# Performance work log

Measured on AMD Instinct MI355X. Metric: run time of the kernel, lower is better.

Reference implementation:

```python
import jax, jax.numpy as jnp
import numpy as np

B, T, F_IN = 256, 168, 128
H = 512            # encoder hidden per direction; decoder hidden = 2H
OUT = 1
L_OUT = 48
SCALE = 0.05


def _lstm_scan(x, Wih, Whh, b, h0, c0):
    # x: [T, B, F]; PyTorch LSTM gate order i, f, g, o
    def step(carry, xt):
        h, c = carry
        g = xt @ Wih.T + h @ Whh.T + b
        i, f, gg, o = jnp.split(g, 4, axis=-1)
        c = jax.nn.sigmoid(f) * c + jax.nn.sigmoid(i) * jnp.tanh(gg)
        h = jax.nn.sigmoid(o) * jnp.tanh(c)
        return (h, c), h
    (hT, cT), ys = jax.lax.scan(step, (h0, c0), x)
    return ys, hT, cT


def setup_inputs() -> dict:
    key = jax.random.key(0)
    ks = jax.random.split(key, 16)
    r = lambda k, shp: (jax.random.normal(k, shp, dtype=jnp.float32) * SCALE)
    return {
        "input_seq": jax.random.normal(ks[0], (B, T, F_IN), dtype=jnp.float32),
        "enc_Wih_f": r(ks[1], (4 * H, F_IN)),
        "enc_Whh_f": r(ks[2], (4 * H, H)),
        "enc_bih_f": r(ks[3], (4 * H,)),
        "enc_bhh_f": r(ks[4], (4 * H,)),
        "enc_Wih_b": r(ks[5], (4 * H, F_IN)),
        "enc_Whh_b": r(ks[6], (4 * H, H)),
        "enc_bih_b": r(ks[7], (4 * H,)),
        "enc_bhh_b": r(ks[8], (4 * H,)),
        "dec_Wih": r(ks[9], (4 * 2 * H, OUT)),
        "dec_Whh": r(ks[10], (4 * 2 * H, 2 * H)),
        "dec_bih": r(ks[11], (4 * 2 * H,)),
        "dec_bhh": r(ks[12], (4 * 2 * H,)),
        "fc_W": r(ks[13], (OUT, 2 * H)),
        "fc_b": r(ks[14], (OUT,)),
        "output_length": L_OUT,
    }


def reference(input_seq, enc_Wih_f, enc_Whh_f, enc_bih_f, enc_bhh_f,
              enc_Wih_b, enc_Whh_b, enc_bih_b, enc_bhh_b,
              dec_Wih, dec_Whh, dec_bih, dec_bhh, fc_W, fc_b, output_length):
    b = input_seq.shape[0]
    h = enc_Whh_f.shape[1]
    x = jnp.transpose(input_seq, (1, 0, 2))  # [T, B, F]
    h0 = jnp.zeros((b, h), input_seq.dtype)
    c0 = jnp.zeros((b, h), input_seq.dtype)
    # bidirectional encoder (final hidden/cell only are used downstream)
    _, hf, cf = _lstm_scan(x, enc_Wih_f, enc_Whh_f, enc_bih_f + enc_bhh_f, h0, c0)
    _, hb, cb = _lstm_scan(x[::-1], enc_Wih_b, enc_Whh_b, enc_bih_b + enc_bhh_b, h0, c0)
    # _cat_hidden: concat fwd/bwd states along feature dim -> decoder init state [B, 2H]
    hd = jnp.concatenate([hf, hb], axis=-1)
    cd = jnp.concatenate([cf, cb], axis=-1)
    bd = dec_bih + dec_bhh
    x0 = jnp.zeros((b, fc_W.shape[0]), input_seq.dtype)  # initial decoder input = zeros

    def dec_step(carry, _):
        hh, cc, xt = carry
        g = xt @ dec_Wih.T + hh @ dec_Whh.T + bd
        i, f, gg, o = jnp.split(g, 4, axis=-1)
        cc = jax.nn.sigmoid(f) * cc + jax.nn.sigmoid(i) * jnp.tanh(gg)
        hh = jax.nn.sigmoid(o) * jnp.tanh(cc)
        pred = hh @ fc_W.T + fc_b  # [B, OUT]
        return (hh, cc, pred), pred

    _, preds = jax.lax.scan(dec_step, (hd, cd, x0), None, length=output_length)
    # [L, B, OUT] -> [B, L, OUT] -> squeeze(dim=2) with OUT==1 -> [B, L]
    return jnp.transpose(preds, (1, 0, 2)).squeeze(2)
```

## Files before the change

### kernel.cpp

```cpp
#include <hip/hip_runtime.h>


constexpr int B_ = 256, T_ = 168, F_ = 128, H_ = 512, L_ = 48;
constexpr int KE = F_ + H_;
constexpr int HD = 1024;
constexpr int GE = 4 * H_;
constexpr int GD = 4 * HD;
constexpr int EPAD = KE + 8;
constexpr int DPAD = HD + 8;

constexpr int GBAR_IDX = 0;
constexpr int CLAIM_IDX = 64;
constexpr int ENCF_IDX = 640;
constexpr int DECF_IDX = 1280;

constexpr size_t OFF_SYNC = 0;
constexpr size_t OFF_WCF = 8192;
constexpr size_t OFF_WCB = OFF_WCF + (size_t)GE * KE * 2;
constexpr size_t OFF_WD  = OFF_WCB + (size_t)GE * KE * 2;
constexpr size_t OFF_BF  = OFF_WD  + (size_t)GD * HD * 2;
constexpr size_t OFF_BB  = OFF_BF  + (size_t)GE * 4;
constexpr size_t OFF_BD  = OFF_BB  + (size_t)GE * 4;
constexpr size_t OFF_WIH = OFF_BD  + (size_t)GD * 4;
constexpr size_t OFF_XH  = OFF_WIH + (size_t)GD * 4;
constexpr size_t OFF_HE  = OFF_XH  + (size_t)T_ * B_ * F_ * 2;
constexpr size_t OFF_HDD = OFF_HE  + (size_t)2 * 2 * B_ * H_ * 2;
constexpr size_t OFF_CD  = OFF_HDD + (size_t)2 * B_ * HD * 2;

using h8 = __attribute__((ext_vector_type(8))) _Float16;
using f4 = __attribute__((ext_vector_type(4))) float;

#define DEV static __device__ __forceinline__

DEV float sigm(float x)  { return __fdividef(1.f, 1.f + __expf(-x)); }
DEV float tanh_(float x) { return 1.f - __fdividef(2.f, __expf(2.f * x) + 1.f); }

DEV h8 as_h8(f4 v) { union { f4 f; h8 h; } u; u.f = v; return u.h; }

DEV void astore_u64(void* p, unsigned long long v) {
  __hip_atomic_store((unsigned long long*)p, v, __ATOMIC_RELAXED,
                     __HIP_MEMORY_SCOPE_AGENT);
}
DEV void astore_u32(void* p, unsigned v) {
  __hip_atomic_store((unsigned*)p, v, __ATOMIC_RELAXED, __HIP_MEMORY_SCOPE_AGENT);
}
DEV unsigned aload_u32(const void* p) {
  return __hip_atomic_load((const unsigned*)p, __ATOMIC_RELAXED,
                           __HIP_MEMORY_SCOPE_AGENT);
}
DEV float aload_f32(const void* p) {
  return __hip_atomic_load((const float*)p, __ATOMIC_RELAXED,
                           __HIP_MEMORY_SCOPE_AGENT);
}
DEV void astore_f32(void* p, float v) {
  __hip_atomic_store((float*)p, v, __ATOMIC_RELAXED, __HIP_MEMORY_SCOPE_AGENT);
}
DEV void vm_drain() { asm volatile("s_waitcnt vmcnt(0)" ::: "memory"); }

template<bool DEEP>
DEV void ld16(const _Float16* p, f4* A) {
#define L16(FL) asm volatile( \
    "global_load_dwordx4 %0,  %16, off" FL "\n\t" \
    "global_load_dwordx4 %1,  %16, off offset:64" FL "\n\t" \
    "global_load_dwordx4 %2,  %16, off offset:128" FL "\n\t" \
    "global_load_dwordx4 %3,  %16, off offset:192" FL "\n\t" \
    "global_load_dwordx4 %4,  %16, off offset:256" FL "\n\t" \
    "global_load_dwordx4 %5,  %16, off offset:320" FL "\n\t" \
    "global_load_dwordx4 %6,  %16, off offset:384" FL "\n\t" \
    "global_load_dwordx4 %7,  %16, off offset:448" FL "\n\t" \
    "global_load_dwordx4 %8,  %16, off offset:512" FL "\n\t" \
    "global_load_dwordx4 %9,  %16, off offset:576" FL "\n\t" \
    "global_load_dwordx4 %10, %16, off offset:640" FL "\n\t" \
    "global_load_dwordx4 %11, %16, off offset:704" FL "\n\t" \
    "global_load_dwordx4 %12, %16, off offset:768" FL "\n\t" \
    "global_load_dwordx4 %13, %16, off offset:832" FL "\n\t" \
    "global_load_dwordx4 %14, %16, off offset:896" FL "\n\t" \
    "global_load_dwordx4 %15, %16, off offset:960" FL "\n\t" \
    "s_waitcnt vmcnt(0)" \
    : "=&v"(A[0]),"=&v"(A[1]),"=&v"(A[2]),"=&v"(A[3]),"=&v"(A[4]),"=&v"(A[5]), \
      "=&v"(A[6]),"=&v"(A[7]),"=&v"(A[8]),"=&v"(A[9]),"=&v"(A[10]),"=&v"(A[11]), \
      "=&v"(A[12]),"=&v"(A[13]),"=&v"(A[14]),"=&v"(A[15]) \
    : "v"(p) : "memory")
  if constexpr (DEEP) { L16(" sc0 sc1"); } else { L16(" sc0"); }
#undef L16
}

DEV void ld32(const _Float16* p, f4* A) {
  asm volatile(
    "global_load_dwordx4 %0,  %32, off sc0 sc1\n\t"
    "global_load_dwordx4 %1,  %32, off offset:64 sc0 sc1\n\t"
    "global_load_dwordx4 %2,  %32, off offset:128 sc0 sc1\n\t"
    "global_load_dwordx4 %3,  %32, off offset:192 sc0 sc1\n\t"
    "global_load_dwordx4 %4,  %32, off offset:256 sc0 sc1\n\t"
    "global_load_dwordx4 %5,  %32, off offset:320 sc0 sc1\n\t"
    "global_load_dwordx4 %6,  %32, off offset:384 sc0 sc1\n\t"
    "global_load_dwordx4 %7,  %32, off offset:448 sc0 sc1\n\t"
    "global_load_dwordx4 %8,  %32, off offset:512 sc0 sc1\n\t"
    "global_load_dwordx4 %9,  %32, off offset:576 sc0 sc1\n\t"
    "global_load_dwordx4 %10, %32, off offset:640 sc0 sc1\n\t"
    "global_load_dwordx4 %11, %32, off offset:704 sc0 sc1\n\t"
    "global_load_dwordx4 %12, %32, off offset:768 sc0 sc1\n\t"
    "global_load_dwordx4 %13, %32, off offset:832 sc0 sc1\n\t"
    "global_load_dwordx4 %14, %32, off offset:896 sc0 sc1\n\t"
    "global_load_dwordx4 %15, %32, off offset:960 sc0 sc1\n\t"
    "global_load_dwordx4 %16, %32, off offset:1024 sc0 sc1\n\t"
    "global_load_dwordx4 %17, %32, off offset:1088 sc0 sc1\n\t"
    "global_load_dwordx4 %18, %32, off offset:1152 sc0 sc1\n\t"
    "global_load_dwordx4 %19, %32, off offset:1216 sc0 sc1\n\t"
    "global_load_dwordx4 %20, %32, off offset:1280 sc0 sc1\n\t"
    "global_load_dwordx4 %21, %32, off offset:1344 sc0 sc1\n\t"
    "global_load_dwordx4 %22, %32, off offset:1408 sc0 sc1\n\t"
    "global_load_dwordx4 %23, %32, off offset:1472 sc0 sc1\n\t"
    "global_load_dwordx4 %24, %32, off offset:1536 sc0 sc1\n\t"
    "global_load_dwordx4 %25, %32, off offset:1600 sc0 sc1\n\t"
    "global_load_dwordx4 %26, %32, off offset:1664 sc0 sc1\n\t"
    "global_load_dwordx4 %27, %32, off offset:1728 sc0 sc1\n\t"
    "global_load_dwordx4 %28, %32, off offset:1792 sc0 sc1\n\t"
    "global_load_dwordx4 %29, %32, off offset:1856 sc0 sc1\n\t"
    "global_load_dwordx4 %30, %32, off offset:1920 sc0 sc1\n\t"
    "global_load_dwordx4 %31, %32, off offset:1984 sc0 sc1\n\t"
    "s_waitcnt vmcnt(0)"
    : "=&v"(A[0]),"=&v"(A[1]),"=&v"(A[2]),"=&v"(A[3]),"=&v"(A[4]),"=&v"(A[5]),
      "=&v"(A[6]),"=&v"(A[7]),"=&v"(A[8]),"=&v"(A[9]),"=&v"(A[10]),"=&v"(A[11]),
      "=&v"(A[12]),"=&v"(A[13]),"=&v"(A[14]),"=&v"(A[15]),"=&v"(A[16]),"=&v"(A[17]),
      "=&v"(A[18]),"=&v"(A[19]),"=&v"(A[20]),"=&v"(A[21]),"=&v"(A[22]),"=&v"(A[23]),
      "=&v"(A[24]),"=&v"(A[25]),"=&v"(A[26]),"=&v"(A[27]),"=&v"(A[28]),"=&v"(A[29]),
      "=&v"(A[30]),"=&v"(A[31])
    : "v"(p) : "memory");
}

DEV unsigned pollflag(const unsigned* p, bool deep) {
  unsigned v;
  if (deep)
    asm volatile("global_load_dword %0, %1, off sc0 sc1\n\t"
                 "s_waitcnt vmcnt(0)" : "=&v"(v) : "v"(p) : "memory");
  else
    asm volatile("global_load_dword %0, %1, off sc0\n\t"
                 "s_waitcnt vmcnt(0)" : "=&v"(v) : "v"(p) : "memory");
  return v;
}
DEV void wait_ge(const unsigned* p, unsigned target, bool deep, int cap) {
  for (int it = 0; it < cap; ++it) {
    unsigned v = pollflag(p, deep);
    if (__ballot(v >= target) == ~0ull) return;
  }
}

DEV void global_sync(unsigned* cnt, unsigned target) {
  vm_drain();
  __syncthreads();
  if (threadIdx.x == 0) {
    __hip_atomic_fetch_add(cnt, 1u, __ATOMIC_RELAXED, __HIP_MEMORY_SCOPE_AGENT);
    for (int it = 0; it < (1 << 20); ++it) {
      if (aload_u32(cnt) >= target) break;
    }
  }
  __syncthreads();
  asm volatile("" ::: "memory");
}

__global__ void prep_misc(const float* bihF, const float* bhhF,
                          const float* bihB, const float* bhhB,
                          const float* dbih, const float* dbhh,
                          const float* dwih, const float* fcb,
                          float* out, char* ws) {
  int i = blockIdx.x * blockDim.x + threadIdx.x;
  if (i < 1024) astore_u64(ws + (size_t)i * 8, 0ull);
  if (i < GE) {
    ((float*)(ws + OFF_BF))[i] = bihF[i] + bhhF[i];
    ((float*)(ws + OFF_BB))[i] = bihB[i] + bhhB[i];
  }
  if (i < GD) {
    ((float*)(ws + OFF_BD))[i]  = dbih[i] + dbhh[i];
    ((float*)(ws + OFF_WIH))[i] = dwih[i];
  }
  if (i < B_ * L_) out[i] = fcb[0];
  if (i < 2 * 2 * B_ * H_ / 4) astore_u64((char*)ws + OFF_HE + (size_t)i * 8, 0ull);
}

__global__ void conv_encw(const float* WihF, const float* WhhF,
                          const float* WihB, const float* WhhB, char* ws) {
  int i = blockIdx.x * blockDim.x + threadIdx.x;
  if (i >= GE * KE) return;
  int r = i / KE, k = i - r * KE;
  float vF = (k < F_) ? WihF[r * F_ + k] : WhhF[r * H_ + (k - F_)];
  float vB = (k < F_) ? WihB[r * F_ + k] : WhhB[r * H_ + (k - F_)];
  ((_Float16*)(ws + OFF_WCF))[i] = (_Float16)vF;
  ((_Float16*)(ws + OFF_WCB))[i] = (_Float16)vB;
}

__global__ void conv_decw(const float* W, char* ws) {
  int i = blockIdx.x * blockDim.x + threadIdx.x;
  if (i < GD * HD) ((_Float16*)(ws + OFF_WD))[i] = (_Float16)W[i];
}

__global__ void conv_x(const float* x, char* ws) {
  int i = blockIdx.x * blockDim.x + threadIdx.x;
  if (i >= T_ * B_ * F_) return;
  int f = i & 127, b = (i >> 7) & 255, t = i >> 15;
  ((_Float16*)(ws + OFF_XH))[i] = (_Float16)x[((size_t)b * T_ + t) * F_ + f];
}

template<bool LOCAL>
DEV void encoder_phase(int dir, int chunk, int slice,
                       int tid, int wave, int quad, int col, int lane,
                       char* ws, _Float16* lds, _Float16 (*htile)[16]) {
  const _Float16* Wenc  = (const _Float16*)(ws + (dir ? OFF_WCB : OFF_WCF));
  const float*    biasE = (const float*)(ws + (dir ? OFF_BB : OFF_BF));
  const _Float16* Xh    = (const _Float16*)(ws + OFF_XH);
  _Float16* hE = (_Float16*)(ws + OFF_HE);
  _Float16* hD = (_Float16*)(ws + OFF_HDD);
  float*    cD = (float*)(ws + OFF_CD);
  unsigned* encf = (unsigned*)ws + ENCF_IDX + (dir * 4 + chunk) * 64;

  const int j0 = slice * 16;
  const int mb = chunk * 64;

  for (int it = 0; it < 20; ++it) {
    int idx = it * 256 + tid;
    int n = idx / 80, e = idx - n * 80;
    int g = n >> 4, u = n & 15;
    *((h8*)(lds + n * EPAD) + e) =
        *((const h8*)(Wenc + (size_t)(g * H_ + j0 + u) * KE) + e);
  }
  float breg[4];
#pragma unroll
  for (int g = 0; g < 4; ++g) breg[g] = biasE[g * H_ + j0 + col];
  float cst[4] = {0.f, 0.f, 0.f, 0.f};
  __syncthreads();

  h8 Bf[4][16];
#pragma unroll
  for (int g = 0; g < 4; ++g)
#pragma unroll
    for (int kk = 0; kk < 16; ++kk)
      Bf[g][kk] = *((const h8*)(lds + (g * 16 + col) * EPAD + F_) + kk * 4 + quad);

  const int arow = mb + wave * 16 + col;
  const int mrow = mb + wave * 16 + quad * 4;

  for (int t = 0; t < T_; ++t) {
    const int par = t & 1;
    const int tx  = dir ? (T_ - 1 - t) : t;
    f4 z = {0.f, 0.f, 0.f, 0.f};
    f4 acc[4] = {z, z, z, z};

    const h8* xr = (const h8*)(Xh + ((size_t)tx * B_ + arow) * F_);
#pragma unroll
    for (int kk = 0; kk < 4; ++kk) {
      h8 a = xr[kk * 4 + quad];
#pragma unroll
      for (int g = 0; g < 4; ++g) {
        h8 b = *((const h8*)(lds + (g * 16 + col) * EPAD) + kk * 4 + quad);
        acc[g] = __builtin_amdgcn_mfma_f32_16x16x32_f16(a, b, acc[g], 0, 0, 0);
      }
    }
    if (t > 0)
      wait_ge(encf + (lane & 31), (unsigned)t, !LOCAL, 1 << 16);
    f4 A[16];
    ld16<!LOCAL>(hE + ((size_t)(par * 2 + dir) * B_ + arow) * H_ + quad * 8, A);
#pragma unroll
    for (int kk = 0; kk < 16; ++kk) {
      h8 a = as_h8(A[kk]);
#pragma unroll
      for (int g = 0; g < 4; ++g)
        acc[g] = __builtin_amdgcn_mfma_f32_16x16x32_f16(a, Bf[g][kk], acc[g], 0, 0, 0);
    }

#pragma unroll
    for (int r = 0; r < 4; ++r) {
      float gi = acc[0][r] + breg[0];
      float gf = acc[1][r] + breg[1];
      float gg = acc[2][r] + breg[2];
      float go = acc[3][r] + breg[3];
      float c = sigm(gf) * cst[r] + sigm(gi) * tanh_(gg);
      cst[r] = c;
      float h = sigm(go) * tanh_(c);
      htile[wave * 16 + quad * 4 + r][col] = (_Float16)h;
      if (t == T_ - 1)
        astore_f32(&cD[(size_t)(mrow + r) * HD + dir * H_ + j0 + col], c);
    }
    __syncthreads();
    if (tid < 128) {
      int row = tid >> 1, half = tid & 1;
      const unsigned long long* src =
          (const unsigned long long*)&htile[row][half * 8];
      if (t < T_ - 1) {
        _Float16* dst = hE + ((size_t)((par ^ 1) * 2 + dir) * B_ + mb + row) * H_ +
                        j0 + half * 8;
        if (LOCAL) {
          ((unsigned long long*)dst)[0] = src[0];
          ((unsigned long long*)(dst + 4))[0] = src[1];
        } else {
          astore_u64(dst, src[0]);
          astore_u64(dst + 4, src[1]);
        }
      } else {
        _Float16* dst = hD + (size_t)(mb + row) * HD + dir * H_ + j0 + half * 8;
        astore_u64(dst, src[0]);
        astore_u64(dst + 4, src[1]);
      }
    }
    vm_drain();
    __syncthreads();
    if (tid == 0 && t < T_ - 1) {
      if (LOCAL) *(volatile unsigned*)(encf + slice) = (unsigned)(t + 1);
      else       astore_u32(encf + slice, (unsigned)(t + 1));
    }
  }
}

DEV void decoder_phase(int slice, int chunk,
                       int tid, int wave, int quad, int col, int lane,
                       const float* fcW, float* out, char* ws,
                       _Float16* lds, _Float16 (*htile)[16]) {
  const _Float16* Wd    = (const _Float16*)(ws + OFF_WD);
  const float*    biasD = (const float*)(ws + OFF_BD);
  const float*    wihD  = (const float*)(ws + OFF_WIH);
  _Float16* hD = (_Float16*)(ws + OFF_HDD);
  float*    cD = (float*)(ws + OFF_CD);
  unsigned* decf = (unsigned*)ws + DECF_IDX + chunk * 64;

  const int j0 = slice * 16;
  const int mb = chunk * 64;

  for (int it = 0; it < 32; ++it) {
    int idx = it * 256 + tid;
    int n = idx >> 7, e = idx & 127;
    int g = n >> 4, u = n & 15;
    *((h8*)(lds + n * DPAD) + e) =
        *((const h8*)(Wd + (size_t)(g * HD + j0 + u) * HD) + e);
  }
  float breg[4], wreg[4];
#pragma unroll
  for (int g = 0; g < 4; ++g) {
    breg[g] = biasD[g * HD + j0 + col];
    wreg[g] = wihD[g * HD + j0 + col];
  }
  const float fcw = fcW[j0 + col];
  const int arow = mb + wave * 16 + col;
  const int mrow = mb + wave * 16 + quad * 4;
  float cst[4];
#pragma unroll
  for (int r = 0; r < 4; ++r)
    cst[r] = aload_f32(&cD[(size_t)(mrow + r) * HD + j0 + col]);
  __syncthreads();

  for (int l = 0; l < L_; ++l) {
    const int par = l & 1;
    if (l > 0) wait_ge(decf + lane, (unsigned)l, true, 1 << 16);
    f4 A[32];
    ld32(hD + ((size_t)par * B_ + arow) * HD + quad * 8, A);
    f4 z = {0.f, 0.f, 0.f, 0.f};
    f4 acc[4] = {z, z, z, z};
#pragma unroll
    for (int kk = 0; kk < 32; ++kk) {
      h8 a = as_h8(A[kk]);
#pragma unroll
      for (int g = 0; g < 4; ++g) {
        h8 b = *((const h8*)(lds + (g * 16 + col) * DPAD) + kk * 4 + quad);
        acc[g] = __builtin_amdgcn_mfma_f32_16x16x32_f16(a, b, acc[g], 0, 0, 0);
      }
    }
    float pr[4];
#pragma unroll
    for (int r = 0; r < 4; ++r)
      pr[r] = (l > 0) ? aload_f32(&out[(size_t)(mrow + r) * L_ + (l - 1)]) : 0.f;

    float sum[4];
#pragma unroll
    for (int r = 0; r < 4; ++r) {
      float gi = acc[0][r] + breg[0] + pr[r] * wreg[0];
      float gf = acc[1][r] + breg[1] + pr[r] * wreg[1];
      float gg = acc[2][r] + breg[2] + pr[r] * wreg[2];
      float go = acc[3][r] + breg[3] + pr[r] * wreg[3];
      float c = sigm(gf) * cst[r] + sigm(gi) * tanh_(gg);
      cst[r] = c;
      float h = sigm(go) * tanh_(c);
      htile[wave * 16 + quad * 4 + r][col] = (_Float16)h;
      sum[r] = h * fcw;
    }
#pragma unroll
    for (int off = 1; off < 16; off <<= 1) {
#pragma unroll
      for (int r = 0; r < 4; ++r) sum[r] += __shfl_xor(sum[r], off, 16);
    }
    if (col == 0) {
#pragma unroll
      for (int r = 0; r < 4; ++r)
        atomicAdd(&out[(size_t)(mrow + r) * L_ + l], sum[r]);
    }
    __syncthreads();
    if (l < L_ - 1 && tid < 128) {
      int row = tid >> 1, half = tid & 1;
      const unsigned long long* src =
          (const unsigned long long*)&htile[row][half * 8];
      _Float16* dst = hD + ((size_t)(par ^ 1) * B_ + mb + row) * HD +
                      j0 + half * 8;
      astore_u64(dst, src[0]);
      astore_u64(dst + 4, src[1]);
    }
    vm_drain();
    __syncthreads();
    if (tid == 0 && l < L_ - 1) astore_u32(decf + slice, (unsigned)(l + 1));
  }
}

__global__ __launch_bounds__(256, 1)
void rnn_kernel(const float* __restrict__ fcW, float* __restrict__ out,
                char* __restrict__ ws) {
  __shared__ __align__(16) _Float16 lds[64 * DPAD];
  __shared__ __align__(16) _Float16 htile[64][16];
  __shared__ int sh[2];

  const int tid  = threadIdx.x;
  const int wave = tid >> 6;
  const int lane = tid & 63;
  const int quad = lane >> 4;
  const int col  = lane & 15;
  const int bi   = blockIdx.x;

  unsigned* sync = (unsigned*)(ws + OFF_SYNC);
  unsigned* gbar = sync + GBAR_IDX;
  unsigned* claim = sync + CLAIM_IDX;

  if (tid == 0) {
    unsigned x;
    asm volatile("s_getreg_b32 %0, hwreg(HW_REG_XCC_ID)" : "=s"(x));
    int xcd = (int)(x & 7u);
    unsigned r = __hip_atomic_fetch_add(claim + xcd * 64, 1u, __ATOMIC_RELAXED,
                                        __HIP_MEMORY_SCOPE_AGENT);
    sh[0] = xcd;
    sh[1] = (int)r;
  }
  __syncthreads();
  const int xcd = sh[0], rank = sh[1];
  global_sync(gbar, 256u);
  if (tid == 0) {
    int d = 0;
    for (int k = 0; k < 8; ++k)
      if (aload_u32(claim + k * 64) != 32u) d = 1;
    sh[0] = d;
  }
  __syncthreads();
  const bool deg = (sh[0] != 0) || (rank >= 32);

  if (!deg)
    encoder_phase<true>(xcd >> 2, xcd & 3, rank, tid, wave, quad, col, lane,
                        ws, lds, htile);
  else
    encoder_phase<false>(bi >> 7, bi & 3, (bi & 127) >> 2, tid, wave, quad, col,
                         lane, ws, lds, htile);

  global_sync(gbar, 512u);

  decoder_phase(bi >> 2, bi & 3, tid, wave, quad, col, lane, fcW, out, ws, lds,
                htile);
}

extern "C" void kernel_launch(void* const* d_in, const int* in_sizes, int n_in,
                              void* d_out, int out_size, void* d_ws, size_t ws_size,
                              hipStream_t stream) {
  const float* x     = (const float*)d_in[0];
  const float* eWihF = (const float*)d_in[1];
  const float* eWhhF = (const float*)d_in[2];
  const float* ebihF = (const float*)d_in[3];
  const float* ebhhF = (const float*)d_in[4];
  const float* eWihB = (const float*)d_in[5];
  const float* eWhhB = (const float*)d_in[6];
  const float* ebihB = (const float*)d_in[7];
  const float* ebhhB = (const float*)d_in[8];
  const float* dWih  = (const float*)d_in[9];
  const float* dWhh  = (const float*)d_in[10];
  const float* dbih  = (const float*)d_in[11];
  const float* dbhh  = (const float*)d_in[12];
  const float* fcW   = (const float*)d_in[13];
  const float* fcb   = (const float*)d_in[14];
  float* out = (float*)d_out;
  char*  ws  = (char*)d_ws;

  prep_misc<<<2048, 256, 0, stream>>>(ebihF, ebhhF, ebihB, ebhhB, dbih, dbhh,
                                      dWih, fcb, out, ws);
  conv_encw<<<(GE * KE) / 256, 256, 0, stream>>>(eWihF, eWhhF, eWihB, eWhhB, ws);
  conv_decw<<<(GD * HD) / 256, 256, 0, stream>>>(dWhh, ws);
  conv_x<<<(T_ * B_ * F_) / 256, 256, 0, stream>>>(x, ws);

  void* args[] = {(void*)&fcW, (void*)&out, (void*)&ws};
  hipError_t err = hipLaunchCooperativeKernel(rnn_kernel, dim3(256), dim3(256),
                                              args, 0, stream);
  if (err != hipSuccess) {
    rnn_kernel<<<dim3(256), dim3(256), 0, stream>>>(fcW, out, ws);
  }
}
```

Measured before the change: 1.478 ms.

## Repartition decoder per XCD with in-register weights and partial-prediction exchange

The decoder is repartitioned so each XCD owns 32 batch rows and each block owns 32 hidden units. Half the gate weights are staged in LDS and half in registers, converted from fp32 inside the kernel, which removes the separate decoder weight conversion kernel and the bias prep. Predictions now come from per-block partial sums in a double-buffered buffer instead of global atomicAdds, and XCD-local flags replace the global per-chunk wait. The grid barrier changes from a shared atomic counter to per-block flags scanned with vector loads. The cost is more register pressure and a larger in-kernel weight load, and the LOCAL (non-coherent) path is never instantiated.

After: 1.476 ms. About the same (-0.2%).

```diff
diff --git a/kernel.cpp b/kernel.cpp
--- a/kernel.cpp
+++ b/kernel.cpp
@@ -5,30 +5,28 @@
 constexpr int KE = F_ + H_;
 constexpr int HD = 1024;
 constexpr int GE = 4 * H_;
-constexpr int GD = 4 * HD;
 constexpr int EPAD = KE + 8;
 constexpr int DPAD = HD + 8;
 
-constexpr int GBAR_IDX = 0;
-constexpr int CLAIM_IDX = 64;
-constexpr int ENCF_IDX = 640;
-constexpr int DECF_IDX = 1280;
+constexpr int FL256_IDX = 0;
+constexpr int CLAIM_IDX = 256;
+constexpr int ENCF_IDX  = 768;
+constexpr int DECF_IDX  = 1280;
 
 constexpr size_t OFF_SYNC = 0;
 constexpr size_t OFF_WCF = 8192;
 constexpr size_t OFF_WCB = OFF_WCF + (size_t)GE * KE * 2;
-constexpr size_t OFF_WD  = OFF_WCB + (size_t)GE * KE * 2;
-constexpr size_t OFF_BF  = OFF_WD  + (size_t)GD * HD * 2;
+constexpr size_t OFF_PP  = OFF_WCB + (size_t)GE * KE * 2;
+constexpr size_t OFF_BF  = OFF_PP  + (size_t)8 * 2 * 64 * 32 * 4;
 constexpr size_t OFF_BB  = OFF_BF  + (size_t)GE * 4;
-constexpr size_t OFF_BD  = OFF_BB  + (size_t)GE * 4;
-constexpr size_t OFF_WIH = OFF_BD  + (size_t)GD * 4;
-constexpr size_t OFF_XH  = OFF_WIH + (size_t)GD * 4;
+constexpr size_t OFF_XH  = OFF_BB  + (size_t)GE * 4;
 constexpr size_t OFF_HE  = OFF_XH  + (size_t)T_ * B_ * F_ * 2;
 constexpr size_t OFF_HDD = OFF_HE  + (size_t)2 * 2 * B_ * H_ * 2;
 constexpr size_t OFF_CD  = OFF_HDD + (size_t)2 * B_ * HD * 2;
 
 using h8 = __attribute__((ext_vector_type(8))) _Float16;
 using f4 = __attribute__((ext_vector_type(4))) float;
+using u4 = __attribute__((ext_vector_type(4))) unsigned;
 
 #define DEV static __device__ __forceinline__
 
@@ -54,6 +52,11 @@
 }
 DEV void astore_f32(void* p, float v) {
   __hip_atomic_store((float*)p, v, __ATOMIC_RELAXED, __HIP_MEMORY_SCOPE_AGENT);
+}
+DEV void astore_u16(void* p, _Float16 v) {
+  union { _Float16 h; unsigned short s; } u; u.h = v;
+  __hip_atomic_store((unsigned short*)p, u.s, __ATOMIC_RELAXED,
+                     __HIP_MEMORY_SCOPE_AGENT);
 }
 DEV void vm_drain() { asm volatile("s_waitcnt vmcnt(0)" ::: "memory"); }
 
@@ -85,48 +88,79 @@
 #undef L16
 }
 
+template<bool DEEP>
 DEV void ld32(const _Float16* p, f4* A) {
-  asm volatile(
-    "global_load_dwordx4 %0,  %32, off sc0 sc1\n\t"
-    "global_load_dwordx4 %1,  %32, off offset:64 sc0 sc1\n\t"
-    "global_load_dwordx4 %2,  %32, off offset:128 sc0 sc1\n\t"
-    "global_load_dwordx4 %3,  %32, off offset:192 sc0 sc1\n\t"
-    "global_load_dwordx4 %4,  %32, off offset:256 sc0 sc1\n\t"
-    "global_load_dwordx4 %5,  %32, off offset:320 sc0 sc1\n\t"
-    "global_load_dwordx4 %6,  %32, off offset:384 sc0 sc1\n\t"
-    "global_load_dwordx4 %7,  %32, off offset:448 sc0 sc1\n\t"
-    "global_load_dwordx4 %8,  %32, off offset:512 sc0 sc1\n\t"
-    "global_load_dwordx4 %9,  %32, off offset:576 sc0 sc1\n\t"
-    "global_load_dwordx4 %10, %32, off offset:640 sc0 sc1\n\t"
-    "global_load_dwordx4 %11, %32, off offset:704 sc0 sc1\n\t"
-    "global_load_dwordx4 %12, %32, off offset:768 sc0 sc1\n\t"
-    "global_load_dwordx4 %13, %32, off offset:832 sc0 sc1\n\t"
-    "global_load_dwordx4 %14, %32, off offset:896 sc0 sc1\n\t"
-    "global_load_dwordx4 %15, %32, off offset:960 sc0 sc1\n\t"
-    "global_load_dwordx4 %16, %32, off offset:1024 sc0 sc1\n\t"
-    "global_load_dwordx4 %17, %32, off offset:1088 sc0 sc1\n\t"
-    "global_load_dwordx4 %18, %32, off offset:1152 sc0 sc1\n\t"
-    "global_load_dwordx4 %19, %32, off offset:1216 sc0 sc1\n\t"
-    "global_load_dwordx4 %20, %32, off offset:1280 sc0 sc1\n\t"
-    "global_load_dwordx4 %21, %32, off offset:1344 sc0 sc1\n\t"
-    "global_load_dwordx4 %22, %32, off offset:1408 sc0 sc1\n\t"
-    "global_load_dwordx4 %23, %32, off offset:1472 sc0 sc1\n\t"
-    "global_load_dwordx4 %24, %32, off offset:1536 sc0 sc1\n\t"
-    "global_load_dwordx4 %25, %32, off offset:1600 sc0 sc1\n\t"
-    "global_load_dwordx4 %26, %32, off offset:1664 sc0 sc1\n\t"
-    "global_load_dwordx4 %27, %32, off offset:1728 sc0 sc1\n\t"
-    "global_load_dwordx4 %28, %32, off offset:1792 sc0 sc1\n\t"
-    "global_load_dwordx4 %29, %32, off offset:1856 sc0 sc1\n\t"
-    "global_load_dwordx4 %30, %32, off offset:1920 sc0 sc1\n\t"
-    "global_load_dwordx4 %31, %32, off offset:1984 sc0 sc1\n\t"
-    "s_waitcnt vmcnt(0)"
-    : "=&v"(A[0]),"=&v"(A[1]),"=&v"(A[2]),"=&v"(A[3]),"=&v"(A[4]),"=&v"(A[5]),
-      "=&v"(A[6]),"=&v"(A[7]),"=&v"(A[8]),"=&v"(A[9]),"=&v"(A[10]),"=&v"(A[11]),
-      "=&v"(A[12]),"=&v"(A[13]),"=&v"(A[14]),"=&v"(A[15]),"=&v"(A[16]),"=&v"(A[17]),
-      "=&v"(A[18]),"=&v"(A[19]),"=&v"(A[20]),"=&v"(A[21]),"=&v"(A[22]),"=&v"(A[23]),
-      "=&v"(A[24]),"=&v"(A[25]),"=&v"(A[26]),"=&v"(A[27]),"=&v"(A[28]),"=&v"(A[29]),
-      "=&v"(A[30]),"=&v"(A[31])
-    : "v"(p) : "memory");
+#define L32(FL) asm volatile( \
+    "global_load_dwordx4 %0,  %32, off" FL "\n\t" \
+    "global_load_dwordx4 %1,  %32, off offset:64" FL "\n\t" \
+    "global_load_dwordx4 %2,  %32, off offset:128" FL "\n\t" \
+    "global_load_dwordx4 %3,  %32, off offset:192" FL "\n\t" \
+    "global_load_dwordx4 %4,  %32, off offset:256" FL "\n\t" \
+    "global_load_dwordx4 %5,  %32, off offset:320" FL "\n\t" \
+    "global_load_dwordx4 %6,  %32, off offset:384" FL "\n\t" \
+    "global_load_dwordx4 %7,  %32, off offset:448" FL "\n\t" \
+    "global_load_dwordx4 %8,  %32, off offset:512" FL "\n\t" \
+    "global_load_dwordx4 %9,  %32, off offset:576" FL "\n\t" \
+    "global_load_dwordx4 %10, %32, off offset:640" FL "\n\t" \
+    "global_load_dwordx4 %11, %32, off offset:704" FL "\n\t" \
+    "global_load_dwordx4 %12, %32, off offset:768" FL "\n\t" \
+    "global_load_dwordx4 %13, %32, off offset:832" FL "\n\t" \
+    "global_load_dwordx4 %14, %32, off offset:896" FL "\n\t" \
+    "global_load_dwordx4 %15, %32, off offset:960" FL "\n\t" \
+    "global_load_dwordx4 %16, %32, off offset:1024" FL "\n\t" \
+    "global_load_dwordx4 %17, %32, off offset:1088" FL "\n\t" \
+    "global_load_dwordx4 %18, %32, off offset:1152" FL "\n\t" \
+    "global_load_dwordx4 %19, %32, off offset:1216" FL "\n\t" \
+    "global_load_dwordx4 %20, %32, off offset:1280" FL "\n\t" \
+    "global_load_dwordx4 %21, %32, off offset:1344" FL "\n\t" \
+    "global_load_dwordx4 %22, %32, off offset:1408" FL "\n\t" \
+    "global_load_dwordx4 %23, %32, off offset:1472" FL "\n\t" \
+    "global_load_dwordx4 %24, %32, off offset:1536" FL "\n\t" \
+    "global_load_dwordx4 %25, %32, off offset:1600" FL "\n\t" \
+    "global_load_dwordx4 %26, %32, off offset:1664" FL "\n\t" \
+    "global_load_dwordx4 %27, %32, off offset:1728" FL "\n\t" \
+    "global_load_dwordx4 %28, %32, off offset:1792" FL "\n\t" \
+    "global_load_dwordx4 %29, %32, off offset:1856" FL "\n\t" \
+    "global_load_dwordx4 %30, %32, off offset:1920" FL "\n\t" \
+    "global_load_dwordx4 %31, %32, off offset:1984" FL "\n\t" \
+    "s_waitcnt vmcnt(0)" \
+    : "=&v"(A[0]),"=&v"(A[1]),"=&v"(A[2]),"=&v"(A[3]),"=&v"(A[4]),"=&v"(A[5]), \
+      "=&v"(A[6]),"=&v"(A[7]),"=&v"(A[8]),"=&v"(A[9]),"=&v"(A[10]),"=&v"(A[11]), \
+      "=&v"(A[12]),"=&v"(A[13]),"=&v"(A[14]),"=&v"(A[15]),"=&v"(A[16]),"=&v"(A[17]), \
+      "=&v"(A[18]),"=&v"(A[19]),"=&v"(A[20]),"=&v"(A[21]),"=&v"(A[22]),"=&v"(A[23]), \
+      "=&v"(A[24]),"=&v"(A[25]),"=&v"(A[26]),"=&v"(A[27]),"=&v"(A[28]),"=&v"(A[29]), \
+      "=&v"(A[30]),"=&v"(A[31]) \
+    : "v"(p) : "memory")
+  if constexpr (DEEP) { L32(" sc0 sc1"); } else { L32(" sc0"); }
+#undef L32
+}
+
+template<bool DEEP>
+DEV void ld16s(const float* p, float* v) {
+#define L16S(FL) asm volatile( \
+    "global_load_dword %0,  %16, off" FL "\n\t" \
+    "global_load_dword %1,  %16, off offset:128" FL "\n\t" \
+    "global_load_dword %2,  %16, off offset:256" FL "\n\t" \
+    "global_load_dword %3,  %16, off offset:384" FL "\n\t" \
+    "global_load_dword %4,  %16, off offset:512" FL "\n\t" \
+    "global_load_dword %5,  %16, off offset:640" FL "\n\t" \
+    "global_load_dword %6,  %16, off offset:768" FL "\n\t" \
+    "global_load_dword %7,  %16, off offset:896" FL "\n\t" \
+    "global_load_dword %8,  %16, off offset:1024" FL "\n\t" \
+    "global_load_dword %9,  %16, off offset:1152" FL "\n\t" \
+    "global_load_dword %10, %16, off offset:1280" FL "\n\t" \
+    "global_load_dword %11, %16, off offset:1408" FL "\n\t" \
+    "global_load_dword %12, %16, off offset:1536" FL "\n\t" \
+    "global_load_dword %13, %16, off offset:1664" FL "\n\t" \
+    "global_load_dword %14, %16, off offset:1792" FL "\n\t" \
+    "global_load_dword %15, %16, off offset:1920" FL "\n\t" \
+    "s_waitcnt vmcnt(0)" \
+    : "=&v"(v[0]),"=&v"(v[1]),"=&v"(v[2]),"=&v"(v[3]),"=&v"(v[4]),"=&v"(v[5]), \
+      "=&v"(v[6]),"=&v"(v[7]),"=&v"(v[8]),"=&v"(v[9]),"=&v"(v[10]),"=&v"(v[11]), \
+      "=&v"(v[12]),"=&v"(v[13]),"=&v"(v[14]),"=&v"(v[15]) \
+    : "v"(p) : "memory")
+  if constexpr (DEEP) { L16S(" sc0 sc1"); } else { L16S(" sc0"); }
+#undef L16S
 }
 
 DEV unsigned pollflag(const unsigned* p, bool deep) {
@@ -146,13 +180,19 @@
   }
 }
 
-DEV void global_sync(unsigned* cnt, unsigned target) {
+DEV void gsync(unsigned* fl, int bi, unsigned phase, int tid) {
   vm_drain();
   __syncthreads();
-  if (threadIdx.x == 0) {
-    __hip_atomic_fetch_add(cnt, 1u, __ATOMIC_RELAXED, __HIP_MEMORY_SCOPE_AGENT);
+  if (tid == 0) astore_u32(fl + bi, phase);
+  if (tid < 64) {
+    const unsigned* p = fl + tid * 4;
     for (int it = 0; it < (1 << 20); ++it) {
-      if (aload_u32(cnt) >= target) break;
+      u4 v;
+      asm volatile("global_load_dwordx4 %0, %1, off sc0 sc1\n\t"
+                   "s_waitcnt vmcnt(0)" : "=&v"(v) : "v"(p) : "memory");
+      unsigned a = v[0] < v[1] ? v[0] : v[1];
+      unsigned b = v[2] < v[3] ? v[2] : v[3];
+      if (__ballot((a < b ? a : b) >= phase) == ~0ull) break;
     }
   }
   __syncthreads();
@@ -160,21 +200,13 @@
 }
 
 __global__ void prep_misc(const float* bihF, const float* bhhF,
-                          const float* bihB, const float* bhhB,
-                          const float* dbih, const float* dbhh,
-                          const float* dwih, const float* fcb,
-                          float* out, char* ws) {
+                          const float* bihB, const float* bhhB, char* ws) {
   int i = blockIdx.x * blockDim.x + threadIdx.x;
   if (i < 1024) astore_u64(ws + (size_t)i * 8, 0ull);
   if (i < GE) {
     ((float*)(ws + OFF_BF))[i] = bihF[i] + bhhF[i];
     ((float*)(ws + OFF_BB))[i] = bihB[i] + bhhB[i];
   }
-  if (i < GD) {
-    ((float*)(ws + OFF_BD))[i]  = dbih[i] + dbhh[i];
-    ((float*)(ws + OFF_WIH))[i] = dwih[i];
-  }
-  if (i < B_ * L_) out[i] = fcb[0];
   if (i < 2 * 2 * B_ * H_ / 4) astore_u64((char*)ws + OFF_HE + (size_t)i * 8, 0ull);
 }
 
@@ -187,11 +219,6 @@
   float vB = (k < F_) ? WihB[r * F_ + k] : WhhB[r * H_ + (k - F_)];
   ((_Float16*)(ws + OFF_WCF))[i] = (_Float16)vF;
   ((_Float16*)(ws + OFF_WCB))[i] = (_Float16)vB;
-}
-
-__global__ void conv_decw(const float* W, char* ws) {
-  int i = blockIdx.x * blockDim.x + threadIdx.x;
-  if (i < GD * HD) ((_Float16*)(ws + OFF_WD))[i] = (_Float16)W[i];
 }
 
 __global__ void conv_x(const float* x, char* ws) {
@@ -310,64 +337,108 @@
   }
 }
 
-DEV void decoder_phase(int slice, int chunk,
-                       int tid, int wave, int quad, int col, int lane,
-                       const float* fcW, float* out, char* ws,
-                       _Float16* lds, _Float16 (*htile)[16]) {
-  const _Float16* Wd    = (const _Float16*)(ws + OFF_WD);
-  const float*    biasD = (const float*)(ws + OFF_BD);
-  const float*    wihD  = (const float*)(ws + OFF_WIH);
-  _Float16* hD = (_Float16*)(ws + OFF_HDD);
-  float*    cD = (float*)(ws + OFF_CD);
-  unsigned* decf = (unsigned*)ws + DECF_IDX + chunk * 64;
-
-  const int j0 = slice * 16;
-  const int mb = chunk * 64;
-
-  for (int it = 0; it < 32; ++it) {
+template<bool LOCAL>
+DEV void decoder_phase(int xcd, int rank, int tid, int wave, int quad, int col,
+                       int lane, const float* dWih, const float* dWhh,
+                       const float* dbih, const float* dbhh, const float* fcW,
+                       const float* fcb, float* out, char* ws, _Float16* lds) {
+  _Float16* hdd = (_Float16*)(ws + OFF_HDD);
+  float* cD = (float*)(ws + OFF_CD);
+  float* PP = (float*)(ws + OFF_PP) + (size_t)xcd * 2 * 64 * 32;
+  unsigned* decf = (unsigned*)ws + DECF_IDX + xcd * 64;
+
+  const int j0b = rank * 32;
+  const int R0  = xcd * 32;
+  const int m   = wave & 1;
+  const int uh  = wave >> 1;
+  const int unit = j0b + uh * 16 + col;
+  const int arow = R0 + m * 16 + col;
+  const int mrow = R0 + m * 16 + quad * 4;
+
+  for (int it = 0; it < 64; ++it) {
     int idx = it * 256 + tid;
-    int n = idx >> 7, e = idx & 127;
-    int g = n >> 4, u = n & 15;
-    *((h8*)(lds + n * DPAD) + e) =
-        *((const h8*)(Wd + (size_t)(g * HD + j0 + u) * HD) + e);
-  }
+    int n = idx >> 8, c = idx & 255;
+    int srow = (n >> 5) * HD + j0b + (n & 31);
+    f4 w = *((const f4*)(dWhh + (size_t)srow * HD + c * 4));
+    union { _Float16 h[4]; unsigned long long q; } u2;
+#pragma unroll
+    for (int i2 = 0; i2 < 4; ++i2) u2.h[i2] = (_Float16)w[i2];
+    *(unsigned long long*)(lds + n * DPAD + c * 4) = u2.q;
+  }
+  h8 Bf[2][32];
+#pragma unroll
+  for (int gg = 0; gg < 2; ++gg)
+#pragma unroll
+    for (int kk = 0; kk < 32; ++kk) {
+      const float* src = dWhh + (size_t)((2 + gg) * HD + unit) * HD + kk * 32 + quad * 8;
+      f4 w0 = *((const f4*)src);
+      f4 w1 = *((const f4*)(src + 4));
+      union { _Float16 h[8]; h8 v; } u3;
+#pragma unroll
+      for (int i2 = 0; i2 < 4; ++i2) {
+        u3.h[i2]     = (_Float16)w0[i2];
+        u3.h[4 + i2] = (_Float16)w1[i2];
+      }
+      Bf[gg][kk] = u3.v;
+    }
   float breg[4], wreg[4];
 #pragma unroll
   for (int g = 0; g < 4; ++g) {
-    breg[g] = biasD[g * HD + j0 + col];
-    wreg[g] = wihD[g * HD + j0 + col];
-  }
-  const float fcw = fcW[j0 + col];
-  const int arow = mb + wave * 16 + col;
-  const int mrow = mb + wave * 16 + quad * 4;
+    breg[g] = dbih[g * HD + unit] + dbhh[g * HD + unit];
+    wreg[g] = dWih[g * HD + unit];
+  }
+  const float fcw = fcW[unit];
+  const float fb  = fcb[0];
   float cst[4];
 #pragma unroll
   for (int r = 0; r < 4; ++r)
-    cst[r] = aload_f32(&cD[(size_t)(mrow + r) * HD + j0 + col]);
+    cst[r] = aload_f32(cD + (size_t)(mrow + r) * HD + unit);
   __syncthreads();
 
-  for (int l = 0; l < L_; ++l) {
+  for (int l = 0; l <= L_; ++l) {
+    float predv = 0.f;
+    if (l > 0) {
+      wait_ge(decf + (lane & 31), (unsigned)l, !LOCAL, 1 << 16);
+      const float* PPr = PP + (size_t)((l - 1) & 1) * 64 * 32;
+      int row = lane & 31, halfsel = lane >> 5;
+      const float* pb = PPr + (size_t)(halfsel * 32) * 32 + row;
+      float pv[16], s = 0.f;
+      ld16s<!LOCAL>(pb, pv);
+#pragma unroll
+      for (int j = 0; j < 16; ++j) s += pv[j];
+      ld16s<!LOCAL>(pb + 16 * 32, pv);
+#pragma unroll
+      for (int j = 0; j < 16; ++j) s += pv[j];
+      s += __shfl_xor(s, 32);
+      predv = s + fb;
+      if (rank == 0 && wave == 0 && lane < 32)
+        astore_f32(out + (size_t)(R0 + lane) * L_ + (l - 1), predv);
+    }
+    if (l == L_) break;
     const int par = l & 1;
-    if (l > 0) wait_ge(decf + lane, (unsigned)l, true, 1 << 16);
+
     f4 A[32];
-    ld32(hD + ((size_t)par * B_ + arow) * HD + quad * 8, A);
+    const _Float16* hsrc = hdd + ((size_t)par * B_ + arow) * HD + quad * 8;
+    if (l == 0 || !LOCAL) ld32<true>(hsrc, A);
+    else                  ld32<false>(hsrc, A);
+
     f4 z = {0.f, 0.f, 0.f, 0.f};
     f4 acc[4] = {z, z, z, z};
 #pragma unroll
     for (int kk = 0; kk < 32; ++kk) {
       h8 a = as_h8(A[kk]);
-#pragma unroll
-      for (int g = 0; g < 4; ++g) {
-        h8 b = *((const h8*)(lds + (g * 16 + col) * DPAD) + kk * 4 + quad);
-        acc[g] = __builtin_amdgcn_mfma_f32_16x16x32_f16(a, b, acc[g], 0, 0, 0);
-      }
-    }
-    float pr[4];
+      h8 b0 = *((const h8*)(lds + (0 * 32 + uh * 16 + col) * DPAD) + kk * 4 + quad);
+      h8 b1 = *((const h8*)(lds + (1 * 32 + uh * 16 + col) * DPAD) + kk * 4 + quad);
+      acc[0] = __builtin_amdgcn_mfma_f32_16x16x32_f16(a, b0, acc[0], 0, 0, 0);
+      acc[1] = __builtin_amdgcn_mfma_f32_16x16x32_f16(a, b1, acc[1], 0, 0, 0);
+      acc[2] = __builtin_amdgcn_mfma_f32_16x16x32_f16(a, Bf[0][kk], acc[2], 0, 0, 0);
+      acc[3] = __builtin_amdgcn_mfma_f32_16x16x32_f16(a, Bf[1][kk], acc[3], 0, 0, 0);
+    }
+
+    float pr[4], sum[4];
 #pragma unroll
     for (int r = 0; r < 4; ++r)
-      pr[r] = (l > 0) ? aload_f32(&out[(size_t)(mrow + r) * L_ + (l - 1)]) : 0.f;
-
-    float sum[4];
+      pr[r] = (l > 0) ? __shfl(predv, m * 16 + quad * 4 + r) : 0.f;
 #pragma unroll
     for (int r = 0; r < 4; ++r) {
       float gi = acc[0][r] + breg[0] + pr[r] * wreg[0];
@@ -377,7 +448,9 @@
       float c = sigm(gf) * cst[r] + sigm(gi) * tanh_(gg);
       cst[r] = c;
       float h = sigm(go) * tanh_(c);
-      htile[wave * 16 + quad * 4 + r][col] = (_Float16)h;
+      size_t hoff = ((size_t)(par ^ 1) * B_ + mrow + r) * HD + unit;
+      if (LOCAL) hdd[hoff] = (_Float16)h;
+      else       astore_u16(hdd + hoff, (_Float16)h);
       sum[r] = h * fcw;
     }
 #pragma unroll
@@ -386,29 +459,33 @@
       for (int r = 0; r < 4; ++r) sum[r] += __shfl_xor(sum[r], off, 16);
     }
     if (col == 0) {
-#pragma unroll
-      for (int r = 0; r < 4; ++r)
-        atomicAdd(&out[(size_t)(mrow + r) * L_ + l], sum[r]);
-    }
-    __syncthreads();
-    if (l < L_ - 1 && tid < 128) {
-      int row = tid >> 1, half = tid & 1;
-      const unsigned long long* src =
-          (const unsigned long long*)&htile[row][half * 8];
-      _Float16* dst = hD + ((size_t)(par ^ 1) * B_ + mb + row) * HD +
-                      j0 + half * 8;
-      astore_u64(dst, src[0]);
-      astore_u64(dst + 4, src[1]);
+      float* PPw = PP + (size_t)(l & 1) * 64 * 32;
+      float* pdst = PPw + (size_t)(rank * 2 + uh) * 32 + m * 16 + quad * 4;
+      if (LOCAL) {
+        f4 v = {sum[0], sum[1], sum[2], sum[3]};
+        *(f4*)pdst = v;
+      } else {
+        union { float f[4]; unsigned long long q[2]; } u5;
+#pragma unroll
+        for (int r = 0; r < 4; ++r) u5.f[r] = sum[r];
+        astore_u64(pdst, u5.q[0]);
+        astore_u64(pdst + 2, u5.q[1]);
+      }
     }
     vm_drain();
     __syncthreads();
-    if (tid == 0 && l < L_ - 1) astore_u32(decf + slice, (unsigned)(l + 1));
+    if (tid == 0) {
+      if (LOCAL) *(volatile unsigned*)(decf + rank) = (unsigned)(l + 1);
+      else       astore_u32(decf + rank, (unsigned)(l + 1));
+    }
   }
 }
 
 __global__ __launch_bounds__(256, 1)
-void rnn_kernel(const float* __restrict__ fcW, float* __restrict__ out,
-                char* __restrict__ ws) {
+void rnn_kernel(const float* __restrict__ dWih, const float* __restrict__ dWhh,
+                const float* __restrict__ dbih, const float* __restrict__ dbhh,
+                const float* __restrict__ fcW, const float* __restrict__ fcb,
+                float* __restrict__ out, char* __restrict__ ws) {
   __shared__ __align__(16) _Float16 lds[64 * DPAD];
   __shared__ __align__(16) _Float16 htile[64][16];
   __shared__ int sh[2];
@@ -420,8 +497,8 @@
   const int col  = lane & 15;
   const int bi   = blockIdx.x;
 
-  unsigned* sync = (unsigned*)(ws + OFF_SYNC);
-  unsigned* gbar = sync + GBAR_IDX;
+  unsigned* sync  = (unsigned*)(ws + OFF_SYNC);
+  unsigned* fl    = sync + FL256_IDX;
   unsigned* claim = sync + CLAIM_IDX;
 
   if (tid == 0) {
@@ -435,7 +512,7 @@
   }
   __syncthreads();
   const int xcd = sh[0], rank = sh[1];
-  global_sync(gbar, 256u);
+  gsync(fl, bi, 1u, tid);
   if (tid == 0) {
     int d = 0;
     for (int k = 0; k < 8; ++k)
@@ -452,10 +529,14 @@
     encoder_phase<false>(bi >> 7, bi & 3, (bi & 127) >> 2, tid, wave, quad, col,
                          lane, ws, lds, htile);
 
-  global_sync(gbar, 512u);
-
-  decoder_phase(bi >> 2, bi & 3, tid, wave, quad, col, lane, fcW, out, ws, lds,
-                htile);
+  gsync(fl, bi, 2u, tid);
+
+  if (!deg)
+    decoder_phase<false>(xcd, rank, tid, wave, quad, col, lane, dWih, dWhh,
+                         dbih, dbhh, fcW, fcb, out, ws, lds);
+  else
+    decoder_phase<false>(bi >> 5, bi & 31, tid, wave, quad, col, lane, dWih,
+                         dWhh, dbih, dbhh, fcW, fcb, out, ws, lds);
 }
 
 extern "C" void kernel_launch(void* const* d_in, const int* in_sizes, int n_in,
@@ -479,16 +560,16 @@
   float* out = (float*)d_out;
   char*  ws  = (char*)d_ws;
 
-  prep_misc<<<2048, 256, 0, stream>>>(ebihF, ebhhF, ebihB, ebhhB, dbih, dbhh,
-                                      dWih, fcb, out, ws);
+  prep_misc<<<512, 256, 0, stream>>>(ebihF, ebhhF, ebihB, ebhhB, ws);
   conv_encw<<<(GE * KE) / 256, 256, 0, stream>>>(eWihF, eWhhF, eWihB, eWhhB, ws);
-  conv_decw<<<(GD * HD) / 256, 256, 0, stream>>>(dWhh, ws);
   conv_x<<<(T_ * B_ * F_) / 256, 256, 0, stream>>>(x, ws);
 
-  void* args[] = {(void*)&fcW, (void*)&out, (void*)&ws};
+  void* args[] = {(void*)&dWih, (void*)&dWhh, (void*)&dbih, (void*)&dbhh,
+                  (void*)&fcW,  (void*)&fcb,  (void*)&out,  (void*)&ws};
   hipError_t err = hipLaunchCooperativeKernel(rnn_kernel, dim3(256), dim3(256),
                                               args, 0, stream);
   if (err != hipSuccess) {
-    rnn_kernel<<<dim3(256), dim3(256), 0, stream>>>(fcW, out, ws);
-  }
-}
+    rnn_kernel<<<dim3(256), dim3(256), 0, stream>>>(dWih, dWhh, dbih, dbhh,
+                                                    fcW, fcb, out, ws);
+  }
+}
```
